# Kernel optimization log

Hardware: AMD Instinct MI355X
Metric: run time of the kernel (lower is better)

Reference implementation:

```python
import jax, jax.numpy as jnp
import numpy as np

N_NODES = 50000
N_EDGES = 800000
IN_FEAT = 256
OUT_FEAT = 256
NUM_RELS = 64
NUM_BASES = 8


def setup_inputs() -> dict:
    key = jax.random.key(0)
    ks = jax.random.split(key, 9)
    x = jax.random.normal(ks[0], (N_NODES, IN_FEAT), dtype=jnp.float32)
    src = jax.random.randint(ks[1], (N_EDGES,), 0, N_NODES, dtype=jnp.int32)
    dst = jax.random.randint(ks[2], (N_EDGES,), 0, N_NODES, dtype=jnp.int32)
    etypes = jax.random.randint(ks[3], (N_EDGES,), 0, NUM_RELS, dtype=jnp.int32)
    norm = jax.random.uniform(ks[4], (N_EDGES, 1), dtype=jnp.float32)
    # glorot-style params
    s_w = (6.0 / (IN_FEAT + OUT_FEAT)) ** 0.5
    weight = jax.random.uniform(ks[5], (NUM_BASES, IN_FEAT, OUT_FEAT), jnp.float32, -s_w, s_w)
    s_c = (6.0 / (NUM_RELS + NUM_BASES)) ** 0.5
    w_comp = jax.random.uniform(ks[6], (NUM_RELS, NUM_BASES), jnp.float32, -s_c, s_c)
    h_bias = jnp.zeros((OUT_FEAT,), jnp.float32)
    loop_weight = jax.random.uniform(ks[7], (IN_FEAT, OUT_FEAT), jnp.float32, -s_w, s_w)
    return {"x": x, "src": src, "dst": dst, "etypes": etypes, "norm": norm,
            "weight": weight, "w_comp": w_comp, "h_bias": h_bias,
            "loop_weight": loop_weight}


def reference(x, src, dst, etypes, norm, weight, w_comp, h_bias, loop_weight):
    # Basis regularizer with num_bases < num_rels:
    #   W_r = sum_b w_comp[r, b] * V_b
    # Per-edge message: msg_e = (x[src_e] @ W_{etype_e}) * norm_e,
    # aggregated by sum onto destination nodes. Since the map is linear,
    # we aggregate per basis first, then apply V_b (8 dense GEMMs).
    n_nodes = x.shape[0]
    coef = w_comp[etypes]                      # [E, B] per-edge basis coeffs
    xs = x[src] * norm                         # [E, D] normalized source feats
    out = jnp.zeros((n_nodes, weight.shape[2]), x.dtype)
    for b in range(weight.shape[0]):           # small fixed loop over bases
        agg = jax.ops.segment_sum(xs * coef[:, b:b + 1], dst,
                                  num_segments=n_nodes)   # [N, D]
        out = out + agg @ weight[b]            # [N, O]
    out = out + h_bias + x @ loop_weight       # bias + self-loop
    return jax.nn.relu(out)
```

## Files before the change

### kernel.cpp

```cpp
#include <hip/hip_runtime.h>
#include <hip/hip_bf16.h>
#include <stdint.h>

#define N_NODES 50000
#define N_EDGES 800000
#define IN_FEAT 256
#define OUT_FEAT 256
#define NUM_RELS 64
#define NUM_BASES 8
#define KTOT 2304
#define MP 50176
#define SCAN_BLKS 196

typedef __attribute__((ext_vector_type(8))) __bf16 bf16x8;
typedef __attribute__((ext_vector_type(4))) __bf16 bf16x4;
typedef __attribute__((ext_vector_type(4))) float f32x4;
typedef __attribute__((ext_vector_type(2))) float f32x2;

__global__ void k_prep(const float* __restrict__ x, __bf16* __restrict__ xb,
                       const int* __restrict__ dst, int* __restrict__ deg,
                       const float* __restrict__ weight, const float* __restrict__ loop_w,
                       __bf16* __restrict__ Wf) {
  int i = blockIdx.x * 256 + threadIdx.x;
  const float4* xp = (const float4*)x;
  float4 u = xp[i * 2], v = xp[i * 2 + 1];
  bf16x8 o;
  o[0] = (__bf16)u.x; o[1] = (__bf16)u.y; o[2] = (__bf16)u.z; o[3] = (__bf16)u.w;
  o[4] = (__bf16)v.x; o[5] = (__bf16)v.y; o[6] = (__bf16)v.z; o[7] = (__bf16)v.w;
  *(bf16x8*)(xb + (size_t)i * 8) = o;
  if (i < N_EDGES) atomicAdd(&deg[dst[i]], 1);
  if (i < 73728) {
    int lane6 = i & 63;
    int F = i >> 6;
    int kt2 = F >> 4;
    int nf = F & 15;
    int oc = nf * 16 + (lane6 & 15);
    int rbase = kt2 * 32 + (lane6 >> 4) * 8;
    bf16x8 w;
#pragma unroll
    for (int j = 0; j < 8; ++j) {
      int r = rbase + j;
      float f = (r < 2048) ? weight[(size_t)r * 256 + oc]
                           : loop_w[(size_t)(r - 2048) * 256 + oc];
      w[j] = (__bf16)f;
    }
    *(bf16x8*)(Wf + (size_t)i * 8) = w;
  }
}

__global__ void k_scan1(const int* __restrict__ deg, int* __restrict__ offs,
                        int* __restrict__ bsum) {
  __shared__ int s[256];
  int t = threadIdx.x;
  int i = blockIdx.x * 256 + t;
  int v = (i < N_NODES) ? deg[i] : 0;
  s[t] = v;
  __syncthreads();
  for (int d = 1; d < 256; d <<= 1) {
    int y = (t >= d) ? s[t - d] : 0;
    __syncthreads();
    s[t] += y;
    __syncthreads();
  }
  if (i < N_NODES) offs[i] = s[t] - v;
  if (t == 255) bsum[blockIdx.x] = s[255];
}

__global__ void k_scan3(int* __restrict__ offs, const int* __restrict__ bsum,
                        int* __restrict__ fill) {
  __shared__ int s[256];
  int t = threadIdx.x;
  s[t] = (t < SCAN_BLKS && t < blockIdx.x) ? bsum[t] : 0;
  __syncthreads();
  for (int d = 128; d; d >>= 1) {
    if (t < d) s[t] += s[t + d];
    __syncthreads();
  }
  int base = s[0];
  int i = blockIdx.x * 256 + t;
  if (i < N_NODES) {
    int o = offs[i] + base;
    offs[i] = o;
    fill[i] = o;
  }
}

__global__ void k_scatter(const int* __restrict__ dst, const int* __restrict__ srcv,
                          const int* __restrict__ ety, const float* __restrict__ norm,
                          int* __restrict__ fill, uint2* __restrict__ erec) {
  int e = blockIdx.x * 256 + threadIdx.x;
  int pos = atomicAdd(&fill[dst[e]], 1);
  erec[pos] = make_uint2((unsigned)srcv[e] | ((unsigned)ety[e] << 16),
                         __float_as_uint(norm[e]));
}

#define AGGE(R, XV, ACC)                                                      \
  do {                                                                        \
    int et_ = __builtin_amdgcn_readfirstlane((int)((R).x >> 16));             \
    float nm_ = __uint_as_float((R).y);                                       \
    f32x2 v0_ = {__uint_as_float((XV).x << 16) * nm_,                         \
                 __uint_as_float((XV).x & 0xffff0000u) * nm_};                 \
    f32x2 v1_ = {__uint_as_float((XV).y << 16) * nm_,                         \
                 __uint_as_float((XV).y & 0xffff0000u) * nm_};                 \
    f32x4 cl_ = *(const f32x4*)(w_comp + et_ * 8);                            \
    f32x4 ch_ = *(const f32x4*)(w_comp + et_ * 8 + 4);                        \
    _Pragma("unroll") for (int b = 0; b < 4; ++b) {                           \
      ACC[b][0] += v0_ * cl_[b];                                              \
      ACC[b][1] += v1_ * cl_[b];                                              \
      ACC[b + 4][0] += v0_ * ch_[b];                                          \
      ACC[b + 4][1] += v1_ * ch_[b];                                          \
    }                                                                         \
  } while (0)

#define EDGE4(RP, I, ACC)                                                     \
  do {                                                                        \
    uint2 r0_ = (RP)[(I) + 0], r1_ = (RP)[(I) + 1];                           \
    uint2 r2_ = (RP)[(I) + 2], r3_ = (RP)[(I) + 3];                           \
    uint2 x0_ = *(const uint2*)(xb + (size_t)(r0_.x & 0xffffu) * IN_FEAT + lo4);\
    uint2 x1_ = *(const uint2*)(xb + (size_t)(r1_.x & 0xffffu) * IN_FEAT + lo4);\
    uint2 x2_ = *(const uint2*)(xb + (size_t)(r2_.x & 0xffffu) * IN_FEAT + lo4);\
    uint2 x3_ = *(const uint2*)(xb + (size_t)(r3_.x & 0xffffu) * IN_FEAT + lo4);\
    AGGE(r0_, x0_, ACC); AGGE(r1_, x1_, ACC);                                 \
    AGGE(r2_, x2_, ACC); AGGE(r3_, x3_, ACC);                                 \
  } while (0)

#define EDGE1(RP, I, ACC)                                                     \
  do {                                                                        \
    uint2 r_ = (RP)[(I)];                                                     \
    uint2 x_ = *(const uint2*)(xb + (size_t)(r_.x & 0xffffu) * IN_FEAT + lo4);\
    AGGE(r_, x_, ACC);                                                        \
  } while (0)

#define WRITE_ROW(ACC, R, NODE)                                               \
  do {                                                                        \
    char* base_ = sA + (size_t)(R) * 128 +                                    \
                  ((((lane >> 1) & 7) ^ ((R) & 7)) * 16 + (lane & 1) * 8);    \
    int ktl_ = lane >> 4;                                                     \
    _Pragma("unroll") for (int b = 0; b < 8; ++b) {                           \
      bf16x4 o_;                                                              \
      o_[0] = (__bf16)ACC[b][0][0]; o_[1] = (__bf16)ACC[b][0][1];             \
      o_[2] = (__bf16)ACC[b][1][0]; o_[3] = (__bf16)ACC[b][1][1];             \
      *(bf16x4*)(base_ + (b * 4 + ktl_) * 4096) = o_;                         \
    }                                                                         \
    uint2 xv_ = ((NODE) < N_NODES)                                            \
        ? *(const uint2*)(xb + (size_t)(NODE) * IN_FEAT + lo4)                \
        : make_uint2(0u, 0u);                                                 \
    *(uint2*)(base_ + (32 + ktl_) * 4096) = xv_;                              \
  } while (0)

#define AGG_PAIR(NA, NB, RA, RB)                                              \
  do {                                                                        \
    f32x2 acca[8][2], accb[8][2];                                             \
    _Pragma("unroll") for (int b = 0; b < 8; ++b) {                           \
      acca[b][0] = f32x2{0.f, 0.f}; acca[b][1] = f32x2{0.f, 0.f};             \
      accb[b][0] = f32x2{0.f, 0.f}; accb[b][1] = f32x2{0.f, 0.f};             \
    }                                                                         \
    int i0a = 0, ca = 0, i0b = 0, cb = 0;                                     \
    if ((NA) < N_NODES) {                                                     \
      i0a = __builtin_amdgcn_readfirstlane(offs[NA]);                         \
      ca  = __builtin_amdgcn_readfirstlane(fin[NA]) - i0a;                    \
    }                                                                         \
    if ((NB) < N_NODES) {                                                     \
      i0b = __builtin_amdgcn_readfirstlane(offs[NB]);                         \
      cb  = __builtin_amdgcn_readfirstlane(fin[NB]) - i0b;                    \
    }                                                                         \
    const uint2* rpa = erec + i0a;                                            \
    const uint2* rpb = erec + i0b;                                            \
    int ia = 0, ib = 0;                                                       \
    int mm = (ca < cb ? ca : cb) & ~3;                                        \
    for (; ia < mm; ia += 4, ib += 4) {                                       \
      EDGE4(rpa, ia, acca);                                                   \
      EDGE4(rpb, ib, accb);                                                   \
    }                                                                         \
    for (; ia + 4 <= ca; ia += 4) EDGE4(rpa, ia, acca);                       \
    for (; ib + 4 <= cb; ib += 4) EDGE4(rpb, ib, accb);                       \
    for (; ia < ca; ++ia) EDGE1(rpa, ia, acca);                               \
    for (; ib < cb; ++ib) EDGE1(rpb, ib, accb);                               \
    WRITE_ROW(acca, RA, NA);                                                  \
    WRITE_ROW(accb, RB, NB);                                                  \
  } while (0)

__global__ __launch_bounds__(1024, 4) void k_fused(
    const __bf16* __restrict__ xb, const float* __restrict__ w_comp,
    const int* __restrict__ offs, const int* __restrict__ fin,
    const uint2* __restrict__ erec, const __bf16* __restrict__ Wf,
    const float* __restrict__ bias, float* __restrict__ out) {
  __shared__ __align__(16) char sA[36 * 4096];

  int t = threadIdx.x;
  int wid = t >> 6, lane = t & 63;
  int tm = blockIdx.x;
  int lo4 = lane * 4;

  {
    int na = tm * 32 + wid * 2;
    AGG_PAIR(na, na + 1, wid * 2, wid * 2 + 1);
  }
  __syncthreads();

  int frow = lane & 15, g = lane >> 4;
  int kb0 = ((g ^ (frow & 7)) << 4);
  int kb1 = (((4 + g) ^ (frow & 7)) << 4);
  const char* ap0 = (const char*)sA + frow * 128;
  const char* ap1 = (const char*)sA + (16 + frow) * 128;

  f32x4 acc2[2];
  acc2[0] = f32x4{0.f, 0.f, 0.f, 0.f};
  acc2[1] = f32x4{0.f, 0.f, 0.f, 0.f};

  bf16x8 Aa[2], Ab[2], B0, B1;

#define LD_A(K2, HALF, D)                                                     \
  do {                                                                        \
    int off_ = ((K2) >> 1) * 4096 + ((HALF) ? kb1 : kb0);                     \
    D[0] = *(const bf16x8*)(ap0 + off_);                                      \
    D[1] = *(const bf16x8*)(ap1 + off_);                                      \
  } while (0)

#define LD_B(K2, D)                                                           \
  do {                                                                        \
    D = *(const bf16x8*)(Wf + (size_t)((K2) * 16 + wid) * 512 + lane * 8);    \
  } while (0)

#define FMA2(AS, BS)                                                          \
  do {                                                                        \
    acc2[0] = __builtin_amdgcn_mfma_f32_16x16x32_bf16(AS[0], BS, acc2[0], 0, 0, 0); \
    acc2[1] = __builtin_amdgcn_mfma_f32_16x16x32_bf16(AS[1], BS, acc2[1], 0, 0, 0); \
  } while (0)

  LD_A(0, 0, Aa); LD_B(0, B0);
  for (int kt = 0; kt < 72; kt += 2) {
    int n1 = kt + 1;
    int n2 = (kt + 2 < 72) ? kt + 2 : 70;
    LD_A(n1, 1, Ab); LD_B(n1, B1); FMA2(Aa, B0);
    LD_A(n2, 0, Aa); LD_B(n2, B0); FMA2(Ab, B1);
  }
#undef LD_A
#undef LD_B
#undef FMA2

  int r0 = (lane >> 4) * 4;
  int c0 = lane & 15;
  int col = wid * 16 + c0;
  float bv = bias[col];
#pragma unroll
  for (int mf = 0; mf < 2; ++mf) {
    int rowb = tm * 32 + mf * 16 + r0;
#pragma unroll
    for (int j = 0; j < 4; ++j) {
      int row = rowb + j;
      if (row < N_NODES) {
        float v = acc2[mf][j] + bv;
        out[(size_t)row * OUT_FEAT + col] = v > 0.f ? v : 0.f;
      }
    }
  }
}

extern "C" void kernel_launch(void* const* d_in, const int* in_sizes, int n_in,
                              void* d_out, int out_size, void* d_ws, size_t ws_size,
                              hipStream_t stream) {
  const float* x      = (const float*)d_in[0];
  const int*   src    = (const int*)d_in[1];
  const int*   dst    = (const int*)d_in[2];
  const int*   ety    = (const int*)d_in[3];
  const float* norm   = (const float*)d_in[4];
  const float* weight = (const float*)d_in[5];
  const float* w_comp = (const float*)d_in[6];
  const float* h_bias = (const float*)d_in[7];
  const float* loop_w = (const float*)d_in[8];
  float* out = (float*)d_out;

  char* ws = (char*)d_ws;
  __bf16* xb = (__bf16*)ws;
  size_t off = (size_t)MP * IN_FEAT * 2;
  __bf16* Wf = (__bf16*)(ws + off);
  off += (size_t)256 * KTOT * 2;
  uint2* erec = (uint2*)(ws + off);
  off += (size_t)N_EDGES * 8;
  int* deg   = (int*)(ws + off);
  int* offs  = deg + N_NODES;
  int* fill  = offs + N_NODES;
  int* bsum  = fill + N_NODES;

  hipMemsetAsync(deg, 0, N_NODES * sizeof(int), stream);
  k_prep<<<(N_NODES * IN_FEAT / 8) / 256, 256, 0, stream>>>(x, xb, dst, deg,
                                                            weight, loop_w, Wf);
  k_scan1<<<SCAN_BLKS, 256, 0, stream>>>(deg, offs, bsum);
  k_scan3<<<SCAN_BLKS, 256, 0, stream>>>(offs, bsum, fill);
  k_scatter<<<N_EDGES / 256, 256, 0, stream>>>(dst, src, ety, norm, fill, erec);
  k_fused<<<MP / 32, 1024, 0, stream>>>(xb, w_comp, offs, fill, erec, Wf, h_bias, out);
}
```

Before: 281.0 us.

## Halve fused block tile to 16 rows with one node per wave

Shrinks each fused block from 32 to 16 destination rows, so every wave aggregates a single node and the GEMM stage issues one MFMA per k-step. The LDS tile is halved and the grid doubled, which should let more blocks reside per CU and improve latency hiding in the gather phase. In exchange, each wave loses the two-node interleave that provided memory-level parallelism, and the basis weights are re-read from global memory twice as often per output row.

```diff
diff --git a/kernel.cpp b/kernel.cpp
--- a/kernel.cpp
+++ b/kernel.cpp
@@ -140,81 +140,58 @@
       bf16x4 o_;                                                              \
       o_[0] = (__bf16)ACC[b][0][0]; o_[1] = (__bf16)ACC[b][0][1];             \
       o_[2] = (__bf16)ACC[b][1][0]; o_[3] = (__bf16)ACC[b][1][1];             \
-      *(bf16x4*)(base_ + (b * 4 + ktl_) * 4096) = o_;                         \
+      *(bf16x4*)(base_ + (b * 4 + ktl_) * 2048) = o_;                         \
     }                                                                         \
     uint2 xv_ = ((NODE) < N_NODES)                                            \
         ? *(const uint2*)(xb + (size_t)(NODE) * IN_FEAT + lo4)                \
         : make_uint2(0u, 0u);                                                 \
-    *(uint2*)(base_ + (32 + ktl_) * 4096) = xv_;                              \
-  } while (0)
-
-#define AGG_PAIR(NA, NB, RA, RB)                                              \
-  do {                                                                        \
-    f32x2 acca[8][2], accb[8][2];                                             \
+    *(uint2*)(base_ + (32 + ktl_) * 2048) = xv_;                              \
+  } while (0)
+
+#define AGG_ONE(NA, RA)                                                       \
+  do {                                                                        \
+    f32x2 acca[8][2];                                                         \
     _Pragma("unroll") for (int b = 0; b < 8; ++b) {                           \
       acca[b][0] = f32x2{0.f, 0.f}; acca[b][1] = f32x2{0.f, 0.f};             \
-      accb[b][0] = f32x2{0.f, 0.f}; accb[b][1] = f32x2{0.f, 0.f};             \
-    }                                                                         \
-    int i0a = 0, ca = 0, i0b = 0, cb = 0;                                     \
+    }                                                                         \
+    int i0a = 0, ca = 0;                                                      \
     if ((NA) < N_NODES) {                                                     \
       i0a = __builtin_amdgcn_readfirstlane(offs[NA]);                         \
       ca  = __builtin_amdgcn_readfirstlane(fin[NA]) - i0a;                    \
     }                                                                         \
-    if ((NB) < N_NODES) {                                                     \
-      i0b = __builtin_amdgcn_readfirstlane(offs[NB]);                         \
-      cb  = __builtin_amdgcn_readfirstlane(fin[NB]) - i0b;                    \
-    }                                                                         \
     const uint2* rpa = erec + i0a;                                            \
-    const uint2* rpb = erec + i0b;                                            \
-    int ia = 0, ib = 0;                                                       \
-    int mm = (ca < cb ? ca : cb) & ~3;                                        \
-    for (; ia < mm; ia += 4, ib += 4) {                                       \
-      EDGE4(rpa, ia, acca);                                                   \
-      EDGE4(rpb, ib, accb);                                                   \
-    }                                                                         \
+    int ia = 0;                                                               \
     for (; ia + 4 <= ca; ia += 4) EDGE4(rpa, ia, acca);                       \
-    for (; ib + 4 <= cb; ib += 4) EDGE4(rpb, ib, accb);                       \
     for (; ia < ca; ++ia) EDGE1(rpa, ia, acca);                               \
-    for (; ib < cb; ++ib) EDGE1(rpb, ib, accb);                               \
     WRITE_ROW(acca, RA, NA);                                                  \
-    WRITE_ROW(accb, RB, NB);                                                  \
-  } while (0)
-
-__global__ __launch_bounds__(1024, 4) void k_fused(
+  } while (0)
+
+__global__ __launch_bounds__(1024, 8) void k_fused(
     const __bf16* __restrict__ xb, const float* __restrict__ w_comp,
     const int* __restrict__ offs, const int* __restrict__ fin,
     const uint2* __restrict__ erec, const __bf16* __restrict__ Wf,
     const float* __restrict__ bias, float* __restrict__ out) {
-  __shared__ __align__(16) char sA[36 * 4096];
+  __shared__ __align__(16) char sA[36 * 2048];
 
   int t = threadIdx.x;
   int wid = t >> 6, lane = t & 63;
   int tm = blockIdx.x;
   int lo4 = lane * 4;
 
-  {
-    int na = tm * 32 + wid * 2;
-    AGG_PAIR(na, na + 1, wid * 2, wid * 2 + 1);
-  }
+  AGG_ONE(tm * 16 + wid, wid);
   __syncthreads();
 
   int frow = lane & 15, g = lane >> 4;
   int kb0 = ((g ^ (frow & 7)) << 4);
   int kb1 = (((4 + g) ^ (frow & 7)) << 4);
   const char* ap0 = (const char*)sA + frow * 128;
-  const char* ap1 = (const char*)sA + (16 + frow) * 128;
-
-  f32x4 acc2[2];
-  acc2[0] = f32x4{0.f, 0.f, 0.f, 0.f};
-  acc2[1] = f32x4{0.f, 0.f, 0.f, 0.f};
-
-  bf16x8 Aa[2], Ab[2], B0, B1;
+
+  f32x4 acc2 = f32x4{0.f, 0.f, 0.f, 0.f};
+  bf16x8 Aa, Ab, B0, B1;
 
 #define LD_A(K2, HALF, D)                                                     \
   do {                                                                        \
-    int off_ = ((K2) >> 1) * 4096 + ((HALF) ? kb1 : kb0);                     \
-    D[0] = *(const bf16x8*)(ap0 + off_);                                      \
-    D[1] = *(const bf16x8*)(ap1 + off_);                                      \
+    D = *(const bf16x8*)(ap0 + ((K2) >> 1) * 2048 + ((HALF) ? kb1 : kb0));    \
   } while (0)
 
 #define LD_B(K2, D)                                                           \
@@ -222,37 +199,31 @@
     D = *(const bf16x8*)(Wf + (size_t)((K2) * 16 + wid) * 512 + lane * 8);    \
   } while (0)
 
-#define FMA2(AS, BS)                                                          \
-  do {                                                                        \
-    acc2[0] = __builtin_amdgcn_mfma_f32_16x16x32_bf16(AS[0], BS, acc2[0], 0, 0, 0); \
-    acc2[1] = __builtin_amdgcn_mfma_f32_16x16x32_bf16(AS[1], BS, acc2[1], 0, 0, 0); \
-  } while (0)
+#define FMA1(AS, BS)                                                          \
+  acc2 = __builtin_amdgcn_mfma_f32_16x16x32_bf16(AS, BS, acc2, 0, 0, 0)
 
   LD_A(0, 0, Aa); LD_B(0, B0);
   for (int kt = 0; kt < 72; kt += 2) {
     int n1 = kt + 1;
     int n2 = (kt + 2 < 72) ? kt + 2 : 70;
-    LD_A(n1, 1, Ab); LD_B(n1, B1); FMA2(Aa, B0);
-    LD_A(n2, 0, Aa); LD_B(n2, B0); FMA2(Ab, B1);
+    LD_A(n1, 1, Ab); LD_B(n1, B1); FMA1(Aa, B0);
+    LD_A(n2, 0, Aa); LD_B(n2, B0); FMA1(Ab, B1);
   }
 #undef LD_A
 #undef LD_B
-#undef FMA2
+#undef FMA1
 
   int r0 = (lane >> 4) * 4;
   int c0 = lane & 15;
   int col = wid * 16 + c0;
   float bv = bias[col];
+  int rowb = tm * 16 + r0;
 #pragma unroll
-  for (int mf = 0; mf < 2; ++mf) {
-    int rowb = tm * 32 + mf * 16 + r0;
-#pragma unroll
-    for (int j = 0; j < 4; ++j) {
-      int row = rowb + j;
-      if (row < N_NODES) {
-        float v = acc2[mf][j] + bv;
-        out[(size_t)row * OUT_FEAT + col] = v > 0.f ? v : 0.f;
-      }
+  for (int j = 0; j < 4; ++j) {
+    int row = rowb + j;
+    if (row < N_NODES) {
+      float v = acc2[j] + bv;
+      out[(size_t)row * OUT_FEAT + col] = v > 0.f ? v : 0.f;
     }
   }
 }
@@ -289,5 +260,5 @@
   k_scan1<<<SCAN_BLKS, 256, 0, stream>>>(deg, offs, bsum);
   k_scan3<<<SCAN_BLKS, 256, 0, stream>>>(offs, bsum, fill);
   k_scatter<<<N_EDGES / 256, 256, 0, stream>>>(dst, src, ety, norm, fill, erec);
-  k_fused<<<MP / 32, 1024, 0, stream>>>(xb, w_comp, offs, fill, erec, Wf, h_bias, out);
-}
+  k_fused<<<MP / 16, 1024, 0, stream>>>(xb, w_comp, offs, fill, erec, Wf, h_bias, out);
+}
```

After: 286.8 us. 1.02x slower.
